# Performance work log

Hardware: AMD Instinct MI355X
Metric: run time of the kernel (lower is better)

The kernel has to match this reference:

```python
import jax, jax.numpy as jnp
import numpy as np

NX, N_IN, N_H1, N_H2, N_O = 65536, 2, 1024, 512, 1


def _deriv_tanh(h):
    # DerivTanh: 4 / (exp(-h^T) + exp(h^T))^2 == sech^2(h)^T, shape [features, nx]
    return 4.0 / (jnp.exp(-h.T) + jnp.exp(h.T)) ** 2


def setup_inputs() -> dict:
    key = jax.random.key(0)
    ks = jax.random.split(key, 7)

    def lin_init(k, fan_in, shape):
        bound = 1.0 / np.sqrt(fan_in)
        return jax.random.uniform(k, shape, jnp.float32, -bound, bound)

    x = jax.random.normal(ks[0], (NX, N_IN), jnp.float32)
    W1 = lin_init(ks[1], N_IN, (N_H1, N_IN))
    b1 = lin_init(ks[2], N_IN, (N_H1,))
    W2 = lin_init(ks[3], N_H1, (N_H2, N_H1))
    b2 = lin_init(ks[4], N_H1, (N_H2,))
    W3 = lin_init(ks[5], N_H2, (N_O, N_H2))
    b3 = lin_init(ks[6], N_H2, (N_O,))
    return {"x": x, "W1": W1, "b1": b1, "W2": W2, "b2": b2, "W3": W3, "b3": b3}


def reference(x, W1, b1, W2, b2, W3, b3):
    # Forward MLP
    h1 = x @ W1.T + b1          # [nx, h1]
    z1 = jnp.tanh(h1)
    h2 = z1 @ W2.T + b2         # [nx, h2]
    z2 = jnp.tanh(h2)
    y = z2 @ W3.T + b3          # [nx, 1]

    # Manual forward-mode derivative chain (transposed layout [features, nx])
    dz1dh1 = _deriv_tanh(h1)    # [h1, nx]
    dz2dh2 = _deriv_tanh(h2)    # [h2, nx]
    dh1dx1 = W1[:, 0][:, None]  # [h1, 1], broadcasts over nx (repeat in original)
    dh1dx2 = W1[:, 1][:, None]  # [h1, 1]

    dydx1 = (W3 @ (dz2dh2 * (W2 @ (dz1dh1 * dh1dx1)))).T  # [nx, 1]
    dydx2 = (W3 @ (dz2dh2 * (W2 @ (dz1dh1 * dh1dx2)))).T  # [nx, 1]

    v1 = dydx2
    v2 = -dydx1
    return (y, v1, v2)
```

## Files before the change

kernel.cpp:

```cpp
#include <hip/hip_runtime.h>


#define NXS    65536
#define SB     32
#define NBLK   2048
#define KSTEPS 16

typedef __attribute__((ext_vector_type(8)))  short bh8_t;
typedef __attribute__((ext_vector_type(16))) float fx16_t;
typedef unsigned int u32;

static __device__ __forceinline__ unsigned short f2bf(float f) {
  u32 u = __builtin_bit_cast(u32, f);
  u += 0x7FFFu + ((u >> 16) & 1u);
  return (unsigned short)(u >> 16);
}

static __device__ __forceinline__ float fast_tanh(float h) {
  float e = __expf(2.0f * h);
  return 1.0f - 2.0f / (e + 1.0f);
}

__global__ void prep_w2t(const float* __restrict__ W2, bh8_t* __restrict__ W2pT) {
  int f = blockIdx.x * 256 + threadIdx.x;
  int col = f & 31;
  int q   = (f >> 5) & 1;
  int nbk = (f >> 6) & 15;
  int kb  = f >> 10;
  const float* row = W2 + (nbk * 32 + col) * 1024 + kb * 16 + 4 * q;
  float4 lo = *(const float4*)(row);
  float4 hi = *(const float4*)(row + 8);
  bh8_t o;
  o[0] = (short)f2bf(lo.x); o[1] = (short)f2bf(lo.y);
  o[2] = (short)f2bf(lo.z); o[3] = (short)f2bf(lo.w);
  o[4] = (short)f2bf(hi.x); o[5] = (short)f2bf(hi.y);
  o[6] = (short)f2bf(hi.z); o[7] = (short)f2bf(hi.w);
  W2pT[f] = o;
}

__global__ __launch_bounds__(256, 2) void fused_kernel(
    const float* __restrict__ x,  const float* __restrict__ W1,
    const float* __restrict__ b1, const float* __restrict__ b2,
    const float* __restrict__ W3, const float* __restrict__ b3,
    const bh8_t* __restrict__ Bg, float* __restrict__ out)
{
  __shared__ __attribute__((aligned(16))) char smem[24576 + 1536];
  const int tid  = threadIdx.x;
  const int lane = tid & 63;
  const int wave = tid >> 6;
  const int q    = lane >> 5;
  const int col  = lane & 31;
  const int s0   = blockIdx.x * SB;

  const int gs  = tid >> 3;
  const int gks = (tid & 7) >> 1;
  const int gqp = tid & 1;
  const float2 xv = *(const float2*)(x + 2 * (s0 + gs));
  const float x0 = xv.x, x1 = xv.y;

  fx16_t acc[3][4];
#pragma unroll
  for (int b = 0; b < 3; ++b)
#pragma unroll
    for (int nb = 0; nb < 4; ++nb)
#pragma unroll
      for (int r = 0; r < 16; ++r) acc[b][nb][r] = 0.0f;

  const int amask = (col & 7) * 16;

  auto stageA = [&](int kt, char* Ab) {
    const int kb = kt * 64 + 16 * gks + 4 * gqp;
    bh8_t vz, va0, va1;
#pragma unroll
    for (int i = 0; i < 8; ++i) {
      int k = kb + (i < 4 ? i : 4 + i);
      float2 w = *(const float2*)(W1 + 2 * k);
      float h = fmaf(x0, w.x, fmaf(x1, w.y, b1[k]));
      float z = fast_tanh(h);
      float d = 1.f - z * z;
      vz[i]  = (short)f2bf(z);
      va0[i] = (short)f2bf(d * w.x);
      va1[i] = (short)f2bf(d * w.y);
    }
    const int uoff = ((2 * gks + gqp) ^ (gs & 7)) * 16;
    *(bh8_t*)(Ab + gs * 128 + uoff)        = vz;
    *(bh8_t*)(Ab + (32 + gs) * 128 + uoff) = va0;
    *(bh8_t*)(Ab + (64 + gs) * 128 + uoff) = va1;
  };

  stageA(0, smem);
  __syncthreads();

  for (int kt = 0; kt < KSTEPS; ++kt) {
    char* Acur = smem + (kt & 1) * 12288;
    char* Anxt = smem + ((kt + 1) & 1) * 12288;
    if (kt + 1 < KSTEPS) stageA(kt + 1, Anxt);
    const int abase = col * 128;
#pragma unroll
    for (int ks = 0; ks < 4; ++ks) {
      const int uoff = ((2 * ks + q) * 16) ^ amask;
      bh8_t a0 = *(const bh8_t*)(Acur + abase + uoff);
      bh8_t a1 = *(const bh8_t*)(Acur + abase + 4096 + uoff);
      bh8_t a2 = *(const bh8_t*)(Acur + abase + 8192 + uoff);
      const int fb = ((4 * kt + ks) * 16 + wave * 4) * 64 + lane;
      bh8_t bf0 = Bg[fb];
      bh8_t bf1 = Bg[fb + 64];
      bh8_t bf2 = Bg[fb + 128];
      bh8_t bf3 = Bg[fb + 192];
      acc[0][0] = __builtin_amdgcn_mfma_f32_32x32x16_bf16(a0, bf0, acc[0][0], 0, 0, 0);
      acc[1][0] = __builtin_amdgcn_mfma_f32_32x32x16_bf16(a1, bf0, acc[1][0], 0, 0, 0);
      acc[2][0] = __builtin_amdgcn_mfma_f32_32x32x16_bf16(a2, bf0, acc[2][0], 0, 0, 0);
      acc[0][1] = __builtin_amdgcn_mfma_f32_32x32x16_bf16(a0, bf1, acc[0][1], 0, 0, 0);
      acc[1][1] = __builtin_amdgcn_mfma_f32_32x32x16_bf16(a1, bf1, acc[1][1], 0, 0, 0);
      acc[2][1] = __builtin_amdgcn_mfma_f32_32x32x16_bf16(a2, bf1, acc[2][1], 0, 0, 0);
      acc[0][2] = __builtin_amdgcn_mfma_f32_32x32x16_bf16(a0, bf2, acc[0][2], 0, 0, 0);
      acc[1][2] = __builtin_amdgcn_mfma_f32_32x32x16_bf16(a1, bf2, acc[1][2], 0, 0, 0);
      acc[2][2] = __builtin_amdgcn_mfma_f32_32x32x16_bf16(a2, bf2, acc[2][2], 0, 0, 0);
      acc[0][3] = __builtin_amdgcn_mfma_f32_32x32x16_bf16(a0, bf3, acc[0][3], 0, 0, 0);
      acc[1][3] = __builtin_amdgcn_mfma_f32_32x32x16_bf16(a1, bf3, acc[1][3], 0, 0, 0);
      acc[2][3] = __builtin_amdgcn_mfma_f32_32x32x16_bf16(a2, bf3, acc[2][3], 0, 0, 0);
    }
    __syncthreads();
  }

  float b2n[4], w3n[4];
#pragma unroll
  for (int nb = 0; nb < 4; ++nb) {
    int n = wave * 128 + nb * 32 + col;
    b2n[nb] = b2[n];
    w3n[nb] = W3[n];
  }
  float* P = (float*)(smem + 24576);
#pragma unroll
  for (int r = 0; r < 16; ++r) {
    const int srow_o = (r & 3) + 8 * (r >> 2) + 4 * q;
    float py = 0.f, p1 = 0.f, p2 = 0.f;
#pragma unroll
    for (int nb = 0; nb < 4; ++nb) {
      float z2 = fast_tanh(acc[0][nb][r] + b2n[nb]);
      float d2 = 1.f - z2 * z2;
      py = fmaf(w3n[nb], z2, py);
      p1 = fmaf(w3n[nb] * d2, acc[1][nb][r], p1);
      p2 = fmaf(w3n[nb] * d2, acc[2][nb][r], p2);
    }
#pragma unroll
    for (int m = 1; m < 32; m <<= 1) {
      py += __shfl_xor(py, m, 64);
      p1 += __shfl_xor(p1, m, 64);
      p2 += __shfl_xor(p2, m, 64);
    }
    if (col == 0) {
      P[0 * 128 + srow_o * 4 + wave] = py;
      P[1 * 128 + srow_o * 4 + wave] = p1;
      P[2 * 128 + srow_o * 4 + wave] = p2;
    }
  }
  __syncthreads();
  if (tid < 96) {
    const int v = tid >> 5, s = tid & 31;
    const float* Pv = P + v * 128 + s * 4;
    float sum = Pv[0] + Pv[1] + Pv[2] + Pv[3];
    const int si = s0 + s;
    if (v == 0)      out[si]           = sum + b3[0];
    else if (v == 2) out[NXS + si]     = sum;
    else             out[2 * NXS + si] = -sum;
  }
}

extern "C" void kernel_launch(void* const* d_in, const int* in_sizes, int n_in,
                              void* d_out, int out_size, void* d_ws, size_t ws_size,
                              hipStream_t stream) {
  const float* x  = (const float*)d_in[0];
  const float* W1 = (const float*)d_in[1];
  const float* b1 = (const float*)d_in[2];
  const float* W2 = (const float*)d_in[3];
  const float* b2 = (const float*)d_in[4];
  const float* W3 = (const float*)d_in[5];
  const float* b3 = (const float*)d_in[6];
  bh8_t* W2pT = (bh8_t*)d_ws;

  prep_w2t<<<256, 256, 0, stream>>>(W2, W2pT);
  fused_kernel<<<NBLK, 256, 0, stream>>>(
      x, W1, b1, b2, W3, b3, (const bh8_t*)W2pT, (float*)d_out);
}
```

Baseline: 289.0 us.

## Double K-tile depth, pack W1/b1 into float4, use packed bf16 converts and MFMA priority

Raises the K tile from 64 to 128 so there are half as many stage/sync iterations, doubling the LDS A buffers to 48KB. It adds a prep step that interleaves W1 and b1 into float4 records so each hidden unit needs one load. It also replaces the scalar bf16 rounding with the packed v_cvt_pk_bf16_f32 instruction and raises wave priority around the MFMA block. The larger LDS footprint may limit occupancy, and the hardware convert may round differently from the manual rounding.

```diff
diff --git a/kernel.cpp b/kernel.cpp
--- a/kernel.cpp
+++ b/kernel.cpp
@@ -4,9 +4,10 @@
 #define NXS    65536
 #define SB     32
 #define NBLK   2048
-#define KSTEPS 16
+#define KSTEPS 8
 
 typedef __attribute__((ext_vector_type(8)))  short bh8_t;
+typedef __attribute__((ext_vector_type(4)))  unsigned int u32x4;
 typedef __attribute__((ext_vector_type(16))) float fx16_t;
 typedef unsigned int u32;
 
@@ -16,12 +17,20 @@
   return (unsigned short)(u >> 16);
 }
 
+static __device__ __forceinline__ u32 pkbf(float lo, float hi) {
+  u32 r;
+  asm("v_cvt_pk_bf16_f32 %0, %1, %2" : "=v"(r) : "v"(lo), "v"(hi));
+  return r;
+}
+
 static __device__ __forceinline__ float fast_tanh(float h) {
   float e = __expf(2.0f * h);
   return 1.0f - 2.0f / (e + 1.0f);
 }
 
-__global__ void prep_w2t(const float* __restrict__ W2, bh8_t* __restrict__ W2pT) {
+__global__ void prep_all(const float* __restrict__ W2, const float* __restrict__ W1,
+                         const float* __restrict__ b1, bh8_t* __restrict__ W2pT,
+                         float4* __restrict__ W1b) {
   int f = blockIdx.x * 256 + threadIdx.x;
   int col = f & 31;
   int q   = (f >> 5) & 1;
@@ -36,15 +45,19 @@
   o[4] = (short)f2bf(hi.x); o[5] = (short)f2bf(hi.y);
   o[6] = (short)f2bf(hi.z); o[7] = (short)f2bf(hi.w);
   W2pT[f] = o;
+  if (f < 1024) {
+    float2 w = *(const float2*)(W1 + 2 * f);
+    W1b[f] = make_float4(w.x, w.y, b1[f], 0.0f);
+  }
 }
 
 __global__ __launch_bounds__(256, 2) void fused_kernel(
-    const float* __restrict__ x,  const float* __restrict__ W1,
-    const float* __restrict__ b1, const float* __restrict__ b2,
-    const float* __restrict__ W3, const float* __restrict__ b3,
-    const bh8_t* __restrict__ Bg, float* __restrict__ out)
+    const float* __restrict__ x,  const float4* __restrict__ W1b,
+    const float* __restrict__ b2, const float* __restrict__ W3,
+    const float* __restrict__ b3, const bh8_t* __restrict__ Bg,
+    float* __restrict__ out)
 {
-  __shared__ __attribute__((aligned(16))) char smem[24576 + 1536];
+  __shared__ __attribute__((aligned(16))) char smem[49152 + 1536];
   const int tid  = threadIdx.x;
   const int lane = tid & 63;
   const int wave = tid >> 6;
@@ -52,11 +65,11 @@
   const int col  = lane & 31;
   const int s0   = blockIdx.x * SB;
 
-  const int gs  = tid >> 3;
-  const int gks = (tid & 7) >> 1;
-  const int gqp = tid & 1;
+  const int gs  = tid & 31;
+  const int gkb = tid >> 5;
   const float2 xv = *(const float2*)(x + 2 * (s0 + gs));
   const float x0 = xv.x, x1 = xv.y;
+  const int wbase = (gs * 256) | (((gkb << 1) ^ (gs & 7)) << 4);
 
   fx16_t acc[3][4];
 #pragma unroll
@@ -66,47 +79,60 @@
 #pragma unroll
       for (int r = 0; r < 16; ++r) acc[b][nb][r] = 0.0f;
 
-  const int amask = (col & 7) * 16;
-
   auto stageA = [&](int kt, char* Ab) {
-    const int kb = kt * 64 + 16 * gks + 4 * gqp;
-    bh8_t vz, va0, va1;
-#pragma unroll
-    for (int i = 0; i < 8; ++i) {
-      int k = kb + (i < 4 ? i : 4 + i);
-      float2 w = *(const float2*)(W1 + 2 * k);
-      float h = fmaf(x0, w.x, fmaf(x1, w.y, b1[k]));
-      float z = fast_tanh(h);
-      float d = 1.f - z * z;
-      vz[i]  = (short)f2bf(z);
-      va0[i] = (short)f2bf(d * w.x);
-      va1[i] = (short)f2bf(d * w.y);
-    }
-    const int uoff = ((2 * gks + gqp) ^ (gs & 7)) * 16;
-    *(bh8_t*)(Ab + gs * 128 + uoff)        = vz;
-    *(bh8_t*)(Ab + (32 + gs) * 128 + uoff) = va0;
-    *(bh8_t*)(Ab + (64 + gs) * 128 + uoff) = va1;
+    const int k16 = kt * 128 + gkb * 16;
+#pragma unroll
+    for (int gqp = 0; gqp < 2; ++gqp) {
+      const int kL = k16 + 4 * gqp;
+      u32x4 wz, wa0, wa1;
+#pragma unroll
+      for (int jp = 0; jp < 2; ++jp) {
+        float4 cA = W1b[kL + 2 * jp];
+        float4 cB = W1b[kL + 2 * jp + 1];
+        float4 cC = W1b[kL + 8 + 2 * jp];
+        float4 cD = W1b[kL + 8 + 2 * jp + 1];
+        float hA = fmaf(x0, cA.x, fmaf(x1, cA.y, cA.z));
+        float hB = fmaf(x0, cB.x, fmaf(x1, cB.y, cB.z));
+        float hC = fmaf(x0, cC.x, fmaf(x1, cC.y, cC.z));
+        float hD = fmaf(x0, cD.x, fmaf(x1, cD.y, cD.z));
+        float zA = fast_tanh(hA), zB = fast_tanh(hB);
+        float zC = fast_tanh(hC), zD = fast_tanh(hD);
+        float dA = 1.f - zA * zA, dB = 1.f - zB * zB;
+        float dC = 1.f - zC * zC, dD = 1.f - zD * zD;
+        wz[jp]      = pkbf(zA, zB);
+        wz[2 + jp]  = pkbf(zC, zD);
+        wa0[jp]     = pkbf(dA * cA.x, dB * cB.x);
+        wa0[2 + jp] = pkbf(dC * cC.x, dD * cD.x);
+        wa1[jp]     = pkbf(dA * cA.y, dB * cB.y);
+        wa1[2 + jp] = pkbf(dC * cC.y, dD * cD.y);
+      }
+      char* dst = Ab + (wbase ^ (gqp << 4));
+      *(u32x4*)(dst)         = wz;
+      *(u32x4*)(dst + 8192)  = wa0;
+      *(u32x4*)(dst + 16384) = wa1;
+    }
   };
 
   stageA(0, smem);
   __syncthreads();
 
   for (int kt = 0; kt < KSTEPS; ++kt) {
-    char* Acur = smem + (kt & 1) * 12288;
-    char* Anxt = smem + ((kt + 1) & 1) * 12288;
+    char* Acur = smem + (kt & 1) * 24576;
+    char* Anxt = smem + ((kt + 1) & 1) * 24576;
     if (kt + 1 < KSTEPS) stageA(kt + 1, Anxt);
-    const int abase = col * 128;
-#pragma unroll
-    for (int ks = 0; ks < 4; ++ks) {
-      const int uoff = ((2 * ks + q) * 16) ^ amask;
+    const int abase = col * 256;
+#pragma unroll
+    for (int ks = 0; ks < 8; ++ks) {
+      const int uoff = (((2 * ks + q) ^ (col & 7)) << 4);
       bh8_t a0 = *(const bh8_t*)(Acur + abase + uoff);
-      bh8_t a1 = *(const bh8_t*)(Acur + abase + 4096 + uoff);
-      bh8_t a2 = *(const bh8_t*)(Acur + abase + 8192 + uoff);
-      const int fb = ((4 * kt + ks) * 16 + wave * 4) * 64 + lane;
+      bh8_t a1 = *(const bh8_t*)(Acur + abase + 8192 + uoff);
+      bh8_t a2 = *(const bh8_t*)(Acur + abase + 16384 + uoff);
+      const int fb = ((kt * 8 + ks) * 16 + wave * 4) * 64 + lane;
       bh8_t bf0 = Bg[fb];
       bh8_t bf1 = Bg[fb + 64];
       bh8_t bf2 = Bg[fb + 128];
       bh8_t bf3 = Bg[fb + 192];
+      __builtin_amdgcn_s_setprio(1);
       acc[0][0] = __builtin_amdgcn_mfma_f32_32x32x16_bf16(a0, bf0, acc[0][0], 0, 0, 0);
       acc[1][0] = __builtin_amdgcn_mfma_f32_32x32x16_bf16(a1, bf0, acc[1][0], 0, 0, 0);
       acc[2][0] = __builtin_amdgcn_mfma_f32_32x32x16_bf16(a2, bf0, acc[2][0], 0, 0, 0);
@@ -119,6 +145,7 @@
       acc[0][3] = __builtin_amdgcn_mfma_f32_32x32x16_bf16(a0, bf3, acc[0][3], 0, 0, 0);
       acc[1][3] = __builtin_amdgcn_mfma_f32_32x32x16_bf16(a1, bf3, acc[1][3], 0, 0, 0);
       acc[2][3] = __builtin_amdgcn_mfma_f32_32x32x16_bf16(a2, bf3, acc[2][3], 0, 0, 0);
+      __builtin_amdgcn_s_setprio(0);
     }
     __syncthreads();
   }
@@ -130,7 +157,7 @@
     b2n[nb] = b2[n];
     w3n[nb] = W3[n];
   }
-  float* P = (float*)(smem + 24576);
+  float* P = (float*)(smem + 49152);
 #pragma unroll
   for (int r = 0; r < 16; ++r) {
     const int srow_o = (r & 3) + 8 * (r >> 2) + 4 * q;
@@ -177,9 +204,10 @@
   const float* b2 = (const float*)d_in[4];
   const float* W3 = (const float*)d_in[5];
   const float* b3 = (const float*)d_in[6];
-  bh8_t* W2pT = (bh8_t*)d_ws;
-
-  prep_w2t<<<256, 256, 0, stream>>>(W2, W2pT);
+  bh8_t*  W2pT = (bh8_t*)d_ws;
+  float4* W1b  = (float4*)((char*)d_ws + (1 << 20));
+
+  prep_all<<<256, 256, 0, stream>>>(W2, W1, b1, W2pT, W1b);
   fused_kernel<<<NBLK, 256, 0, stream>>>(
-      x, W1, b1, b2, W3, b3, (const bh8_t*)W2pT, (float*)d_out);
-}
+      x, W1b, b2, W3, b3, (const bh8_t*)W2pT, (float*)d_out);
+}
```

New measurement: 297.5 us. +2.9%, slower.
